# Optimization experiments

Hardware: AMD Instinct MI355X
Metric: run time of the kernel (lower is better)

The kernel has to match this reference:

```python
import jax, jax.numpy as jnp
import numpy as np

W_SIZE = 7      # window side
TOPK = 8        # top-k windows gathered per query window
D_HEAD = 32     # head dim
EPS = 1e-6      # linear-attention denominator eps


def _windows(x, ws):
    # x: [b, d, H, W] -> [b, (m*n), ws*ws, d]
    b, d, H, W = x.shape
    m, n = H // ws, W // ws
    x = x.reshape(b, d, m, ws, n, ws)
    return x.transpose(0, 2, 4, 3, 5, 1).reshape(b, m * n, ws * ws, d), m, n


def setup_inputs() -> dict:
    key = jax.random.key(0)
    kq, kk, kv = jax.random.split(key, 3)
    shape = (4, 256, 112, 112)
    return {
        "q": jax.random.normal(kq, shape, dtype=jnp.float32),
        "k": jax.random.normal(kk, shape, dtype=jnp.float32),
        "v": jax.random.normal(kv, shape, dtype=jnp.float32),
    }


def reference(q, k, v):
    b, d, H, W = q.shape
    ws = W_SIZE
    qw, m, n = _windows(q, ws)
    kw, _, _ = _windows(k, ws)
    vw, _, _ = _windows(v, ws)
    nw = m * n

    # window mean pooling
    qm = qw.mean(axis=2)  # [b, nw, d]
    km = kw.mean(axis=2)
    vm = vw.mean(axis=2)

    # coarse window similarity + topk
    sim = jnp.einsum('bmd,bnd->bmn', qm, km)
    _, idx = jax.lax.top_k(sim, TOPK)  # [b, nw, TOPK] int32

    # gather fine key/value windows: kw[i][idx[i]] -> [b, nw, TOPK, ws*ws, d]
    gather = jax.vmap(lambda w_, i_: w_[i_])
    fine_k = gather(kw, idx).reshape(b, nw, TOPK * ws * ws, d)
    fine_v = gather(vw, idx).reshape(b, nw, TOPK * ws * ws, d)

    # concat coarse (mean) tokens tiled across query windows
    keys = jnp.concatenate([fine_k, jnp.broadcast_to(km[:, None], (b, nw, nw, d))], axis=2)
    values = jnp.concatenate([fine_v, jnp.broadcast_to(vm[:, None], (b, nw, nw, d))], axis=2)

    h_heads = d // D_HEAD
    L = ws * ws
    S = keys.shape[2]
    Q = qw.reshape(b * nw, L, h_heads, D_HEAD)
    K = keys.reshape(b * nw, S, h_heads, D_HEAD)
    V = values.reshape(b * nw, S, h_heads, D_HEAD)

    # linear attention (elu feature map)
    Qf = jax.nn.elu(Q) + 1.0
    Kf = jax.nn.elu(K) + 1.0
    Vn = V / S
    KV = jnp.einsum('nshd,nshv->nhdv', Kf, Vn)
    Z = 1.0 / (jnp.einsum('nlhd,nhd->nlh', Qf, Kf.sum(axis=1)) + EPS)
    msg = jnp.einsum('nlhd,nhdv,nlh->nlhv', Qf, KV, Z) * S  # [b*nw, L, h, D_HEAD]

    # '(b m n) (w1 w2) h d -> b (h d) (m w1) (n w2)'
    msg = msg.reshape(b, m, n, ws, ws, h_heads, D_HEAD)
    msg = msg.transpose(0, 5, 6, 1, 3, 2, 4).reshape(b, d, m * ws, n * ws)
    return msg
```

## Files before the change

kernel.cpp:

```cpp
#include <hip/hip_runtime.h>
#include <float.h>

#define B 4
#define D 256
#define HH 112
#define WW 112
#define WS 7
#define NW 256
#define LL 49
#define TOPK 8
#define NH 8
#define DH 32
#define PADK 136
#define PADQ 136

typedef unsigned short u16;
typedef unsigned int u32;

__device__ __forceinline__ float elu1(float x) {
    return x > 0.f ? x + 1.f : __expf(x);
}
__device__ __forceinline__ float bf2f(u16 u) {
    return __uint_as_float(((u32)u) << 16);
}
__device__ __forceinline__ u16 f2bf(float x) {
    u32 u = __float_as_uint(x);
    u32 r = (u + 0x7FFFu + ((u >> 16) & 1u)) >> 16;
    return (u16)r;
}

__global__ __launch_bounds__(256) void k_xform(
        const float* __restrict__ q, const float* __restrict__ k,
        const float* __restrict__ v,
        u16* __restrict__ qwin, u16* __restrict__ kwin, u16* __restrict__ vwin,
        float* __restrict__ qm, float* __restrict__ kmf,
        float* __restrict__ vm, float* __restrict__ kmT) {
    __shared__ float stage[16 * 392];
    int blk = blockIdx.x;
    int cg = blk & 15, wjh = (blk >> 4) & 1, wi = (blk >> 5) & 15;
    int b = (blk >> 9) & 3, ti = blk >> 11;
    int c0 = cg * 16;
    int t = threadIdx.x;
    const float* src = ti == 0 ? q : (ti == 1 ? k : v);
    u16* dst = ti == 0 ? qwin : (ti == 1 ? kwin : vwin);

    for (int p = t; p < 1568; p += 256) {
        int c = p / 98;
        int f4 = (p - c * 98) * 4;
        int r = f4 / 56, lcol = f4 - r * 56;
        const float* gp = src +
            ((size_t)((b * D + c0 + c) * HH + wi * WS + r)) * WW + wjh * 56 + lcol;
        *(float4*)&stage[c * 392 + f4] = *(const float4*)gp;
    }
    __syncthreads();

    if (t < 128) {
        int c = t >> 3, wjl = t & 7;
        int base = c * 392 + wjl * 7;
        float s = 0.f;
        for (int r = 0; r < WS; ++r)
            for (int x = 0; x < WS; ++x)
                s += stage[base + r * 56 + x];
        float mean = s * (1.f / 49.f);
        int C = c0 + c;
        int win = wi * 16 + wjh * 8 + wjl;
        if (ti == 0) qm[(size_t)(b * NW + win) * D + C] = mean;
        else if (ti == 1) {
            kmf[(size_t)(b * NW + win) * D + C] = elu1(mean);
            kmT[(size_t)(b * D + C) * NW + win] = mean;
        } else vm[(size_t)(b * NW + win) * D + C] = mean;
    }
    __syncthreads();

    for (int p = t; p < 784; p += 256) {
        int wjl = p / 98;
        int rem = p - wjl * 98;
        int l = rem >> 1, oct = rem & 1;
        int r = l / 7, x = l - r * 7;
        int fo = r * 56 + wjl * 7 + x;
        u32 wds[4];
        for (int h = 0; h < 4; ++h) {
            int cA = oct * 8 + h * 2;
            u16 a  = f2bf(stage[cA * 392 + fo]);
            u16 bq = f2bf(stage[(cA + 1) * 392 + fo]);
            wds[h] = ((u32)bq << 16) | a;
        }
        int win = wi * 16 + wjh * 8 + wjl;
        u16* gp = dst + ((size_t)(b * NW + win) * LL + l) * D + c0 + oct * 8;
        *(uint4*)gp = make_uint4(wds[0], wds[1], wds[2], wds[3]);
    }
}

__global__ __launch_bounds__(256) void k_topk(
        const float* __restrict__ qm, const float* __restrict__ kmT,
        int* __restrict__ idx) {
    __shared__ float qrow[D];
    __shared__ float cval[4];
    __shared__ int cidx[4];
    __shared__ int winner;
    int b = blockIdx.x >> 8;
    int qw = blockIdx.x & 255;
    int t = threadIdx.x;
    qrow[t] = qm[(size_t)(b * NW + qw) * D + t];
    __syncthreads();
    const float* kb = kmT + (size_t)b * D * NW + t;
    float a0 = 0.f, a1 = 0.f, a2 = 0.f, a3 = 0.f;
    for (int d = 0; d < D; d += 4) {
        a0 += qrow[d]     * kb[(size_t)d * NW];
        a1 += qrow[d + 1] * kb[(size_t)(d + 1) * NW];
        a2 += qrow[d + 2] * kb[(size_t)(d + 2) * NW];
        a3 += qrow[d + 3] * kb[(size_t)(d + 3) * NW];
    }
    float val = (a0 + a1) + (a2 + a3);
    for (int sel = 0; sel < TOPK; ++sel) {
        float v = val; int ii = t;
        for (int off = 32; off > 0; off >>= 1) {
            float ov = __shfl_xor(v, off);
            int oi = __shfl_xor(ii, off);
            if (ov > v || (ov == v && oi < ii)) { v = ov; ii = oi; }
        }
        if ((t & 63) == 0) { cval[t >> 6] = v; cidx[t >> 6] = ii; }
        __syncthreads();
        if (t == 0) {
            float bv = cval[0]; int bi = cidx[0];
            for (int w = 1; w < 4; ++w)
                if (cval[w] > bv || (cval[w] == bv && cidx[w] < bi)) {
                    bv = cval[w]; bi = cidx[w];
                }
            idx[(size_t)(b * NW + qw) * TOPK + sel] = bi;
            winner = bi;
        }
        __syncthreads();
        if (t == winner) val = -FLT_MAX;
    }
}

__global__ __launch_bounds__(256) void k_kvw(
        const u16* __restrict__ kwin, const u16* __restrict__ vwin,
        float* __restrict__ KVw, float* __restrict__ Ksw) {
    __shared__ u16 kf[LL * PADK];
    __shared__ u16 vf[LL * PADK];
    int blk = blockIdx.x;
    int b = blk >> 9;
    int win = (blk >> 1) & 255;
    int half = blk & 1;
    int t = threadIdx.x;
    for (int p = t; p < 784; p += 256) {
        int l = p >> 4, oct = p & 15;
        size_t goff = ((size_t)(b * NW + win) * LL + l) * D + half * 128 + oct * 8;
        uint4 raw = *(const uint4*)(kwin + goff);
        u32 w[4] = {raw.x, raw.y, raw.z, raw.w};
        u32 o[4];
        for (int h = 0; h < 4; ++h) {
            float lo = elu1(__uint_as_float(w[h] << 16));
            float hi = elu1(__uint_as_float(w[h] & 0xffff0000u));
            o[h] = ((u32)f2bf(hi) << 16) | f2bf(lo);
        }
        *(uint4*)&kf[l * PADK + oct * 8] = make_uint4(o[0], o[1], o[2], o[3]);
        *(uint4*)&vf[l * PADK + oct * 8] = *(const uint4*)(vwin + goff);
    }
    __syncthreads();
    int h2 = t >> 6;
    int q64 = t & 63;
    int ddq = q64 >> 3, dvq = q64 & 7;
    int ab = h2 * 32 + ddq * 4;
    int bb = h2 * 32 + dvq * 4;
    float acc[4][4] = {};
    float ks[4] = {};
    for (int l = 0; l < LL; ++l) {
        uint2 kr = *(const uint2*)&kf[l * PADK + ab];
        uint2 vr = *(const uint2*)&vf[l * PADK + bb];
        float av[4] = {
            __uint_as_float(kr.x << 16), __uint_as_float(kr.x & 0xffff0000u),
            __uint_as_float(kr.y << 16), __uint_as_float(kr.y & 0xffff0000u)};
        float bw[4] = {
            __uint_as_float(vr.x << 16), __uint_as_float(vr.x & 0xffff0000u),
            __uint_as_float(vr.y << 16), __uint_as_float(vr.y & 0xffff0000u)};
        ks[0] += av[0]; ks[1] += av[1]; ks[2] += av[2]; ks[3] += av[3];
        for (int i = 0; i < 4; ++i)
            for (int j = 0; j < 4; ++j)
                acc[i][j] += av[i] * bw[j];
    }
    int h = half * 4 + h2;
    size_t obase = (size_t)((b * NW + win) * NH + h) * (DH * DH);
    for (int i = 0; i < 4; ++i) {
        float4 o = {acc[i][0], acc[i][1], acc[i][2], acc[i][3]};
        *(float4*)&KVw[obase + (size_t)(ddq * 4 + i) * DH + dvq * 4] = o;
    }
    if (dvq == 0) {
        float4 o = {ks[0], ks[1], ks[2], ks[3]};
        *(float4*)&Ksw[(size_t)((b * NW + win) * NH + h) * DH + ddq * 4] = o;
    }
}

__global__ __launch_bounds__(256) void k_kvc(
        const float* __restrict__ kmf, const float* __restrict__ vm,
        float* __restrict__ KVc, float* __restrict__ Ksc) {
    int b = blockIdx.x >> 1;
    int half = blockIdx.x & 1;
    int t = threadIdx.x;
    int h2 = t >> 6;
    int q64 = t & 63;
    int ddq = q64 >> 3, dvq = q64 & 7;
    int ca = half * 128 + h2 * 32 + ddq * 4;
    int cb = half * 128 + h2 * 32 + dvq * 4;
    const float* kb = kmf + (size_t)b * NW * D;
    const float* vb = vm + (size_t)b * NW * D;
    float acc[4][4] = {};
    float ks[4] = {};
#pragma unroll 4
    for (int n = 0; n < NW; ++n) {
        float4 a  = *(const float4*)&kb[n * D + ca];
        float4 bv = *(const float4*)&vb[n * D + cb];
        float av[4] = {a.x, a.y, a.z, a.w};
        float bw[4] = {bv.x, bv.y, bv.z, bv.w};
        ks[0] += av[0]; ks[1] += av[1]; ks[2] += av[2]; ks[3] += av[3];
        for (int i = 0; i < 4; ++i)
            for (int j = 0; j < 4; ++j)
                acc[i][j] += av[i] * bw[j];
    }
    int h = half * 4 + h2;
    size_t obase = (size_t)(b * NH + h) * (DH * DH);
    for (int i = 0; i < 4; ++i) {
        float4 o = {acc[i][0], acc[i][1], acc[i][2], acc[i][3]};
        *(float4*)&KVc[obase + (size_t)(ddq * 4 + i) * DH + dvq * 4] = o;
    }
    if (dvq == 0) {
        float4 o = {ks[0], ks[1], ks[2], ks[3]};
        *(float4*)&Ksc[(size_t)(b * NH + h) * DH + ddq * 4] = o;
    }
}

__global__ __launch_bounds__(256) void k_final(
        const u16* qwin, const int* __restrict__ idx,
        const float* __restrict__ KVw, const float* __restrict__ Ksw,
        const float* __restrict__ KVc, const float* __restrict__ Ksc,
        u16* msg) {
    __shared__ float kv[4 * DH * DH];
    __shared__ float ksl[4 * DH];
    __shared__ u16 qf[LL * PADQ];
    __shared__ int idxl[TOPK];
    int blk = blockIdx.x;
    int lin = ((blk & 7) << 8) | (blk >> 3);
    int half = lin & 1;
    int qw = (lin >> 1) & 255;
    int b = lin >> 9;
    int t = threadIdx.x;
    if (t < TOPK) idxl[t] = idx[(size_t)(b * NW + qw) * TOPK + t];
    for (int p = t; p < 784; p += 256) {
        int l = p >> 4, oct = p & 15;
        const u16* gp = qwin +
            ((size_t)(b * NW + qw) * LL + l) * D + half * 128 + oct * 8;
        uint4 raw = *(const uint4*)gp;
        u32 wsin[4] = {raw.x, raw.y, raw.z, raw.w};
        u32 wout[4];
        for (int h = 0; h < 4; ++h) {
            float lo = elu1(__uint_as_float(wsin[h] << 16));
            float hi = elu1(__uint_as_float(wsin[h] & 0xffff0000u));
            wout[h] = ((u32)f2bf(hi) << 16) | f2bf(lo);
        }
        *(uint4*)&qf[l * PADQ + oct * 8] = make_uint4(wout[0], wout[1], wout[2], wout[3]);
    }
    __syncthreads();
    {
        int h2 = t >> 6;
        int dd = (t & 63) >> 1;
        int dvh = t & 1;
        int h = half * 4 + h2;
        float kvacc[16] = {};
        float ksacc = 0.f;
        for (int s = 0; s <= TOPK; ++s) {
            const float* kvsrc;
            const float* kssrc;
            if (s < TOPK) {
                int srcw = idxl[s];
                kvsrc = KVw + (size_t)((b * NW + srcw) * NH + h) * (DH * DH);
                kssrc = Ksw + (size_t)((b * NW + srcw) * NH + h) * DH;
            } else {
                kvsrc = KVc + (size_t)(b * NH + h) * (DH * DH);
                kssrc = Ksc + (size_t)(b * NH + h) * DH;
            }
            const float* rowp = kvsrc + (size_t)dd * DH + dvh * 16;
            for (int j4 = 0; j4 < 4; ++j4) {
                float4 r4 = *(const float4*)&rowp[j4 * 4];
                kvacc[j4 * 4 + 0] += r4.x; kvacc[j4 * 4 + 1] += r4.y;
                kvacc[j4 * 4 + 2] += r4.z; kvacc[j4 * 4 + 3] += r4.w;
            }
            ksacc += kssrc[dd];
        }
        for (int j = 0; j < 16; ++j)
            kv[h2 * (DH * DH) + dd * DH + dvh * 16 + j] = kvacc[j];
        if (dvh == 0) ksl[h2 * DH + dd] = ksacc;
    }
    __syncthreads();
    {
        int lset = t >> 7;
        int h2 = (t >> 5) & 3;
        int dv = t & 31;
        float kvcol[DH], ksr[DH];
        for (int dd = 0; dd < DH; ++dd) {
            kvcol[dd] = kv[h2 * (DH * DH) + dd * DH + dv];
            ksr[dd]  = ksl[h2 * DH + dd];
        }
        int l0 = lset * 25;
        int l1 = l0 + 25; if (l1 > LL) l1 = LL;
        for (int l = l0; l < l1; ++l) {
            const u16* qrow = &qf[l * PADQ + h2 * DH];
            float m = 0.f, z = 0.f;
            for (int dd2 = 0; dd2 < 16; ++dd2) {
                u32 w = *(const u32*)&qrow[dd2 * 2];
                float q0 = __uint_as_float(w << 16);
                float q1 = __uint_as_float(w & 0xffff0000u);
                m += q0 * kvcol[2 * dd2] + q1 * kvcol[2 * dd2 + 1];
                z += q0 * ksr[2 * dd2] + q1 * ksr[2 * dd2 + 1];
            }
            qf[l * PADQ + h2 * DH + dv] = f2bf(m / (z + 1e-6f));
        }
    }
    __syncthreads();
    for (int p = t; p < 784; p += 256) {
        int l = p >> 4, oct = p & 15;
        uint4 w = *(const uint4*)&qf[l * PADQ + oct * 8];
        u16* gp = msg + ((size_t)(b * NW + qw) * LL + l) * D + half * 128 + oct * 8;
        *(uint4*)gp = w;
    }
}

__global__ __launch_bounds__(256) void k_out(
        const u16* __restrict__ msg, float* __restrict__ out) {
    __shared__ u16 ms[16 * LL * 32];
    int blk = blockIdx.x;
    int cg = blk & 7, wi = (blk >> 3) & 15, b = blk >> 7;
    int c0 = cg * 32;
    int t = threadIdx.x;
    for (int p = t; p < 3136; p += 256) {
        int wj = p / 196;
        int rem = p - wj * 196;
        int l = rem >> 2, oct = rem & 3;
        const u16* gp = msg +
            ((size_t)(b * NW + wi * 16 + wj) * LL + l) * D + c0 + oct * 8;
        uint4 raw = *(const uint4*)gp;
        *(uint4*)&ms[(wj * LL + l) * 32 + oct * 8] = raw;
    }
    __syncthreads();
    for (int p = t; p < 6272; p += 256) {
        int c = p / 196;
        int rem = p - c * 196;
        int f = rem * 4;
        int r = f / 112, col = f - r * 112;
        float4 o;
        float* op = (float*)&o;
        for (int j = 0; j < 4; ++j) {
            int xg = col + j;
            int wj = xg / 7, x = xg - wj * 7;
            int l = r * 7 + x;
            op[j] = bf2f(ms[(wj * LL + l) * 32 + c]);
        }
        float* gp = out + ((size_t)((b * D + c0 + c) * HH + wi * WS + r)) * WW + col;
        *(float4*)gp = o;
    }
}

extern "C" void kernel_launch(void* const* d_in, const int* in_sizes, int n_in,
                              void* d_out, int out_size, void* d_ws, size_t ws_size,
                              hipStream_t stream) {
    const float* q = (const float*)d_in[0];
    const float* k = (const float*)d_in[1];
    const float* v = (const float*)d_in[2];
    float* out = (float*)d_out;
    char* base = (char*)d_ws;

    float* qm  = (float*)(base);
    float* kmf = (float*)(base + (size_t)1 * (1 << 20));
    float* vm  = (float*)(base + (size_t)2 * (1 << 20));
    float* kmT = (float*)(base + (size_t)3 * (1 << 20));
    int*   idx = (int*)  (base + (size_t)4 * (1 << 20));
    float* Ksw = (float*)(base + (size_t)4 * (1 << 20) + (1 << 15));
    float* KVc = (float*)(base + (size_t)5 * (1 << 20) + (1 << 15));
    float* Ksc = (float*)(base + (size_t)5 * (1 << 20) + (1 << 15) + (1 << 17));
    float* KVw = (float*)(base + (size_t)6 * (1 << 20));
    u16* kwin  = (u16*)(base + (size_t)40 * (1 << 20));
    u16* vwin  = (u16*)(base + (size_t)65 * (1 << 20));
    u16* qwin  = (u16*)(base + (size_t)90 * (1 << 20));

    k_xform<<<dim3(3 * B * 16 * 2 * 16), dim3(256), 0, stream>>>(
        q, k, v, qwin, kwin, vwin, qm, kmf, vm, kmT);
    k_topk <<<dim3(B * NW), dim3(256), 0, stream>>>(qm, kmT, idx);
    k_kvw  <<<dim3(B * NW * 2), dim3(256), 0, stream>>>(kwin, vwin, KVw, Ksw);
    k_kvc  <<<dim3(B * 2), dim3(256), 0, stream>>>(kmf, vm, KVc, Ksc);
    k_final<<<dim3(B * NW * 2), dim3(256), 0, stream>>>(
        qwin, idx, KVw, Ksw, KVc, Ksc, qwin );
    k_out  <<<dim3(B * 16 * 8), dim3(256), 0, stream>>>(qwin, out);
}
```

Measured before the change: 381.5 us.

## Switch window buffers to channel-major layout, fold ELU into transform, merge coarse KV kernel

Window tensors are now stored channel-major ([win][channel][56 padded tokens]) instead of token-major. The ELU feature map is applied once in the transform kernel rather than being recomputed in the KV and final kernels. The coarse KV computation moves into extra blocks of the per-window KV kernel, removing one launch. Per-window KV matrices are stored in bf16 to cut gather traffic in the final kernel. Staging, the final matvec loop and the output scatter are reorganised around the new layout, which adds token padding and some bf16 rounding of the KV sums.

```diff
diff --git a/kernel.cpp b/kernel.cpp
--- a/kernel.cpp
+++ b/kernel.cpp
@@ -8,11 +8,11 @@
 #define WS 7
 #define NW 256
 #define LL 49
+#define LP 56
 #define TOPK 8
 #define NH 8
 #define DH 32
-#define PADK 136
-#define PADQ 136
+#define STK 60
 
 typedef unsigned short u16;
 typedef unsigned int u32;
@@ -28,6 +28,8 @@
     u32 r = (u + 0x7FFFu + ((u >> 16) & 1u)) >> 16;
     return (u16)r;
 }
+__device__ __forceinline__ float bflo(u32 w) { return __uint_as_float(w << 16); }
+__device__ __forceinline__ float bfhi(u32 w) { return __uint_as_float(w & 0xffff0000u); }
 
 __global__ __launch_bounds__(256) void k_xform(
         const float* __restrict__ q, const float* __restrict__ k,
@@ -35,35 +37,32 @@
         u16* __restrict__ qwin, u16* __restrict__ kwin, u16* __restrict__ vwin,
         float* __restrict__ qm, float* __restrict__ kmf,
         float* __restrict__ vm, float* __restrict__ kmT) {
-    __shared__ float stage[16 * 392];
+    __shared__ float stage[8 * 788];
     int blk = blockIdx.x;
-    int cg = blk & 15, wjh = (blk >> 4) & 1, wi = (blk >> 5) & 15;
-    int b = (blk >> 9) & 3, ti = blk >> 11;
-    int c0 = cg * 16;
+    int cg = blk & 31, wi = (blk >> 5) & 15, b = (blk >> 9) & 3, ti = blk >> 11;
+    int c0 = cg * 8;
     int t = threadIdx.x;
     const float* src = ti == 0 ? q : (ti == 1 ? k : v);
     u16* dst = ti == 0 ? qwin : (ti == 1 ? kwin : vwin);
 
     for (int p = t; p < 1568; p += 256) {
-        int c = p / 98;
-        int f4 = (p - c * 98) * 4;
-        int r = f4 / 56, lcol = f4 - r * 56;
-        const float* gp = src +
-            ((size_t)((b * D + c0 + c) * HH + wi * WS + r)) * WW + wjh * 56 + lcol;
-        *(float4*)&stage[c * 392 + f4] = *(const float4*)gp;
+        int c = p / 196;
+        int i4 = (p - c * 196) * 4;
+        const float* gp = src + (size_t)(b * D + c0 + c) * (HH * WW) + wi * 784 + i4;
+        *(float4*)&stage[c * 788 + i4] = *(const float4*)gp;
     }
     __syncthreads();
 
     if (t < 128) {
-        int c = t >> 3, wjl = t & 7;
-        int base = c * 392 + wjl * 7;
+        int c = t >> 4, wjl = t & 15;
+        int base = c * 788 + wjl * 7;
         float s = 0.f;
         for (int r = 0; r < WS; ++r)
             for (int x = 0; x < WS; ++x)
-                s += stage[base + r * 56 + x];
+                s += stage[base + r * 112 + x];
         float mean = s * (1.f / 49.f);
         int C = c0 + c;
-        int win = wi * 16 + wjh * 8 + wjl;
+        int win = wi * 16 + wjl;
         if (ti == 0) qm[(size_t)(b * NW + win) * D + C] = mean;
         else if (ti == 1) {
             kmf[(size_t)(b * NW + win) * D + C] = elu1(mean);
@@ -72,22 +71,25 @@
     }
     __syncthreads();
 
-    for (int p = t; p < 784; p += 256) {
-        int wjl = p / 98;
-        int rem = p - wjl * 98;
-        int l = rem >> 1, oct = rem & 1;
-        int r = l / 7, x = l - r * 7;
-        int fo = r * 56 + wjl * 7 + x;
-        u32 wds[4];
-        for (int h = 0; h < 4; ++h) {
-            int cA = oct * 8 + h * 2;
-            u16 a  = f2bf(stage[cA * 392 + fo]);
-            u16 bq = f2bf(stage[(cA + 1) * 392 + fo]);
-            wds[h] = ((u32)bq << 16) | a;
-        }
-        int win = wi * 16 + wjh * 8 + wjl;
-        u16* gp = dst + ((size_t)(b * NW + win) * LL + l) * D + c0 + oct * 8;
-        *(uint4*)gp = make_uint4(wds[0], wds[1], wds[2], wds[3]);
+    for (int p = t; p < 896; p += 256) {
+        int wjl = p / 56;
+        int rem = p - wjl * 56;
+        int c = rem / 7, j = rem % 7;
+        u16 vals[8];
+        for (int i = 0; i < 8; ++i) {
+            int l = j * 8 + i;
+            if (l < LL) {
+                int r = l / 7, x = l - r * 7;
+                float f = stage[c * 788 + r * 112 + wjl * 7 + x];
+                if (ti < 2) f = elu1(f);
+                vals[i] = f2bf(f);
+            } else vals[i] = 0;
+        }
+        int win = wi * 16 + wjl;
+        u16* gp = dst + ((size_t)(b * NW + win) * D + c0 + c) * LP + j * 8;
+        *(uint4*)gp = make_uint4(
+            ((u32)vals[1] << 16) | vals[0], ((u32)vals[3] << 16) | vals[2],
+            ((u32)vals[5] << 16) | vals[4], ((u32)vals[7] << 16) | vals[6]);
     }
 }
 
@@ -137,55 +139,88 @@
 
 __global__ __launch_bounds__(256) void k_kvw(
         const u16* __restrict__ kwin, const u16* __restrict__ vwin,
-        float* __restrict__ KVw, float* __restrict__ Ksw) {
-    __shared__ u16 kf[LL * PADK];
-    __shared__ u16 vf[LL * PADK];
+        const float* __restrict__ kmf, const float* __restrict__ vm,
+        u16* __restrict__ KVw, float* __restrict__ Ksw,
+        float* __restrict__ KVc, float* __restrict__ Ksc) {
+    __shared__ u16 kf[128 * STK];
+    __shared__ u16 vf[128 * STK];
     int blk = blockIdx.x;
+    int t = threadIdx.x;
+    if (blk >= B * NW * 2) {
+        int blkc = blk - B * NW * 2;
+        int b = blkc >> 1, half = blkc & 1;
+        int h2 = t >> 6, q64 = t & 63, ddq = q64 >> 3, dvq = q64 & 7;
+        int ca = half * 128 + h2 * 32 + ddq * 4;
+        int cb = half * 128 + h2 * 32 + dvq * 4;
+        const float* kb = kmf + (size_t)b * NW * D;
+        const float* vb = vm + (size_t)b * NW * D;
+        float acc[4][4] = {};
+        float ks[4] = {};
+        for (int n = 0; n < NW; ++n) {
+            float4 a  = *(const float4*)&kb[n * D + ca];
+            float4 bv = *(const float4*)&vb[n * D + cb];
+            float av[4] = {a.x, a.y, a.z, a.w};
+            float bw[4] = {bv.x, bv.y, bv.z, bv.w};
+            ks[0] += av[0]; ks[1] += av[1]; ks[2] += av[2]; ks[3] += av[3];
+            for (int i = 0; i < 4; ++i)
+                for (int j = 0; j < 4; ++j)
+                    acc[i][j] += av[i] * bw[j];
+        }
+        int h = half * 4 + h2;
+        size_t obase = (size_t)(b * NH + h) * (DH * DH);
+        for (int i = 0; i < 4; ++i) {
+            float4 o = {acc[i][0], acc[i][1], acc[i][2], acc[i][3]};
+            *(float4*)&KVc[obase + (size_t)(ddq * 4 + i) * DH + dvq * 4] = o;
+        }
+        if (dvq == 0) {
+            float4 o = {ks[0], ks[1], ks[2], ks[3]};
+            *(float4*)&Ksc[(size_t)(b * NH + h) * DH + ddq * 4] = o;
+        }
+        return;
+    }
     int b = blk >> 9;
     int win = (blk >> 1) & 255;
     int half = blk & 1;
-    int t = threadIdx.x;
-    for (int p = t; p < 784; p += 256) {
-        int l = p >> 4, oct = p & 15;
-        size_t goff = ((size_t)(b * NW + win) * LL + l) * D + half * 128 + oct * 8;
-        uint4 raw = *(const uint4*)(kwin + goff);
-        u32 w[4] = {raw.x, raw.y, raw.z, raw.w};
-        u32 o[4];
-        for (int h = 0; h < 4; ++h) {
-            float lo = elu1(__uint_as_float(w[h] << 16));
-            float hi = elu1(__uint_as_float(w[h] & 0xffff0000u));
-            o[h] = ((u32)f2bf(hi) << 16) | f2bf(lo);
-        }
-        *(uint4*)&kf[l * PADK + oct * 8] = make_uint4(o[0], o[1], o[2], o[3]);
-        *(uint4*)&vf[l * PADK + oct * 8] = *(const uint4*)(vwin + goff);
-    }
-    __syncthreads();
-    int h2 = t >> 6;
-    int q64 = t & 63;
-    int ddq = q64 >> 3, dvq = q64 & 7;
-    int ab = h2 * 32 + ddq * 4;
-    int bb = h2 * 32 + dvq * 4;
+    const u16* kg = kwin + ((size_t)(b * NW + win) * D + half * 128) * LP;
+    const u16* vg = vwin + ((size_t)(b * NW + win) * D + half * 128) * LP;
+    for (int p = t; p < 896; p += 256) {
+        int c = p / 7, j = p % 7;
+        uint4 kq = *(const uint4*)(kg + c * LP + j * 8);
+        uint4 vq = *(const uint4*)(vg + c * LP + j * 8);
+        *(uint2*)&kf[c * STK + j * 8]     = make_uint2(kq.x, kq.y);
+        *(uint2*)&kf[c * STK + j * 8 + 4] = make_uint2(kq.z, kq.w);
+        *(uint2*)&vf[c * STK + j * 8]     = make_uint2(vq.x, vq.y);
+        *(uint2*)&vf[c * STK + j * 8 + 4] = make_uint2(vq.z, vq.w);
+    }
+    __syncthreads();
+    int h2 = t >> 6, q64 = t & 63, ddq = q64 >> 3, dvq = q64 & 7;
+    const u16* ka = kf + (h2 * 32 + ddq * 4) * STK;
+    const u16* vb = vf + (h2 * 32 + dvq * 4) * STK;
     float acc[4][4] = {};
     float ks[4] = {};
-    for (int l = 0; l < LL; ++l) {
-        uint2 kr = *(const uint2*)&kf[l * PADK + ab];
-        uint2 vr = *(const uint2*)&vf[l * PADK + bb];
-        float av[4] = {
-            __uint_as_float(kr.x << 16), __uint_as_float(kr.x & 0xffff0000u),
-            __uint_as_float(kr.y << 16), __uint_as_float(kr.y & 0xffff0000u)};
-        float bw[4] = {
-            __uint_as_float(vr.x << 16), __uint_as_float(vr.x & 0xffff0000u),
-            __uint_as_float(vr.y << 16), __uint_as_float(vr.y & 0xffff0000u)};
-        ks[0] += av[0]; ks[1] += av[1]; ks[2] += av[2]; ks[3] += av[3];
-        for (int i = 0; i < 4; ++i)
+    for (int l4 = 0; l4 < 14; ++l4) {
+        float a[4][4], w[4][4];
+        for (int i = 0; i < 4; ++i) {
+            uint2 kr = *(const uint2*)(ka + i * STK + l4 * 4);
+            a[i][0] = bflo(kr.x); a[i][1] = bfhi(kr.x);
+            a[i][2] = bflo(kr.y); a[i][3] = bfhi(kr.y);
+            uint2 vr = *(const uint2*)(vb + i * STK + l4 * 4);
+            w[i][0] = bflo(vr.x); w[i][1] = bfhi(vr.x);
+            w[i][2] = bflo(vr.y); w[i][3] = bfhi(vr.y);
+        }
+        for (int i = 0; i < 4; ++i) {
+            ks[i] += (a[i][0] + a[i][1]) + (a[i][2] + a[i][3]);
             for (int j = 0; j < 4; ++j)
-                acc[i][j] += av[i] * bw[j];
+                for (int s = 0; s < 4; ++s)
+                    acc[i][j] += a[i][s] * w[j][s];
+        }
     }
     int h = half * 4 + h2;
-    size_t obase = (size_t)((b * NW + win) * NH + h) * (DH * DH);
+    u16* ob = KVw + (size_t)((b * NW + win) * NH + h) * (DH * DH);
     for (int i = 0; i < 4; ++i) {
-        float4 o = {acc[i][0], acc[i][1], acc[i][2], acc[i][3]};
-        *(float4*)&KVw[obase + (size_t)(ddq * 4 + i) * DH + dvq * 4] = o;
+        u32 p0 = ((u32)f2bf(acc[i][1]) << 16) | f2bf(acc[i][0]);
+        u32 p1 = ((u32)f2bf(acc[i][3]) << 16) | f2bf(acc[i][2]);
+        *(uint2*)(ob + (ddq * 4 + i) * DH + dvq * 4) = make_uint2(p0, p1);
     }
     if (dvq == 0) {
         float4 o = {ks[0], ks[1], ks[2], ks[3]};
@@ -193,52 +228,14 @@
     }
 }
 
-__global__ __launch_bounds__(256) void k_kvc(
-        const float* __restrict__ kmf, const float* __restrict__ vm,
-        float* __restrict__ KVc, float* __restrict__ Ksc) {
-    int b = blockIdx.x >> 1;
-    int half = blockIdx.x & 1;
-    int t = threadIdx.x;
-    int h2 = t >> 6;
-    int q64 = t & 63;
-    int ddq = q64 >> 3, dvq = q64 & 7;
-    int ca = half * 128 + h2 * 32 + ddq * 4;
-    int cb = half * 128 + h2 * 32 + dvq * 4;
-    const float* kb = kmf + (size_t)b * NW * D;
-    const float* vb = vm + (size_t)b * NW * D;
-    float acc[4][4] = {};
-    float ks[4] = {};
-#pragma unroll 4
-    for (int n = 0; n < NW; ++n) {
-        float4 a  = *(const float4*)&kb[n * D + ca];
-        float4 bv = *(const float4*)&vb[n * D + cb];
-        float av[4] = {a.x, a.y, a.z, a.w};
-        float bw[4] = {bv.x, bv.y, bv.z, bv.w};
-        ks[0] += av[0]; ks[1] += av[1]; ks[2] += av[2]; ks[3] += av[3];
-        for (int i = 0; i < 4; ++i)
-            for (int j = 0; j < 4; ++j)
-                acc[i][j] += av[i] * bw[j];
-    }
-    int h = half * 4 + h2;
-    size_t obase = (size_t)(b * NH + h) * (DH * DH);
-    for (int i = 0; i < 4; ++i) {
-        float4 o = {acc[i][0], acc[i][1], acc[i][2], acc[i][3]};
-        *(float4*)&KVc[obase + (size_t)(ddq * 4 + i) * DH + dvq * 4] = o;
-    }
-    if (dvq == 0) {
-        float4 o = {ks[0], ks[1], ks[2], ks[3]};
-        *(float4*)&Ksc[(size_t)(b * NH + h) * DH + ddq * 4] = o;
-    }
-}
-
 __global__ __launch_bounds__(256) void k_final(
         const u16* qwin, const int* __restrict__ idx,
-        const float* __restrict__ KVw, const float* __restrict__ Ksw,
+        const u16* __restrict__ KVw, const float* __restrict__ Ksw,
         const float* __restrict__ KVc, const float* __restrict__ Ksc,
         u16* msg) {
     __shared__ float kv[4 * DH * DH];
     __shared__ float ksl[4 * DH];
-    __shared__ u16 qf[LL * PADQ];
+    __shared__ u16 qf[128 * LP];
     __shared__ int idxl[TOPK];
     int blk = blockIdx.x;
     int lin = ((blk & 7) << 8) | (blk >> 3);
@@ -247,20 +244,9 @@
     int b = lin >> 9;
     int t = threadIdx.x;
     if (t < TOPK) idxl[t] = idx[(size_t)(b * NW + qw) * TOPK + t];
-    for (int p = t; p < 784; p += 256) {
-        int l = p >> 4, oct = p & 15;
-        const u16* gp = qwin +
-            ((size_t)(b * NW + qw) * LL + l) * D + half * 128 + oct * 8;
-        uint4 raw = *(const uint4*)gp;
-        u32 wsin[4] = {raw.x, raw.y, raw.z, raw.w};
-        u32 wout[4];
-        for (int h = 0; h < 4; ++h) {
-            float lo = elu1(__uint_as_float(wsin[h] << 16));
-            float hi = elu1(__uint_as_float(wsin[h] & 0xffff0000u));
-            wout[h] = ((u32)f2bf(hi) << 16) | f2bf(lo);
-        }
-        *(uint4*)&qf[l * PADQ + oct * 8] = make_uint4(wout[0], wout[1], wout[2], wout[3]);
-    }
+    const u16* qg = qwin + ((size_t)(b * NW + qw) * D + half * 128) * LP;
+    for (int p = t; p < 896; p += 256)
+        *(uint4*)&qf[p * 8] = *(const uint4*)(qg + p * 8);
     __syncthreads();
     {
         int h2 = t >> 6;
@@ -269,24 +255,33 @@
         int h = half * 4 + h2;
         float kvacc[16] = {};
         float ksacc = 0.f;
-        for (int s = 0; s <= TOPK; ++s) {
-            const float* kvsrc;
-            const float* kssrc;
-            if (s < TOPK) {
-                int srcw = idxl[s];
-                kvsrc = KVw + (size_t)((b * NW + srcw) * NH + h) * (DH * DH);
-                kssrc = Ksw + (size_t)((b * NW + srcw) * NH + h) * DH;
-            } else {
-                kvsrc = KVc + (size_t)(b * NH + h) * (DH * DH);
-                kssrc = Ksc + (size_t)(b * NH + h) * DH;
+        for (int s = 0; s < TOPK; ++s) {
+            int srcw = idxl[s];
+            const u16* rp = KVw + (size_t)((b * NW + srcw) * NH + h) * (DH * DH)
+                            + dd * DH + dvh * 16;
+            uint4 r0 = *(const uint4*)rp;
+            uint4 r1 = *(const uint4*)(rp + 8);
+            u32 wsv[4] = {r0.x, r0.y, r0.z, r0.w};
+            for (int h4 = 0; h4 < 4; ++h4) {
+                kvacc[h4 * 2]     += bflo(wsv[h4]);
+                kvacc[h4 * 2 + 1] += bfhi(wsv[h4]);
             }
-            const float* rowp = kvsrc + (size_t)dd * DH + dvh * 16;
+            u32 wsv1[4] = {r1.x, r1.y, r1.z, r1.w};
+            for (int h4 = 0; h4 < 4; ++h4) {
+                kvacc[8 + h4 * 2]     += bflo(wsv1[h4]);
+                kvacc[8 + h4 * 2 + 1] += bfhi(wsv1[h4]);
+            }
+            ksacc += Ksw[(size_t)((b * NW + srcw) * NH + h) * DH + dd];
+        }
+        {
+            const float* rowp = KVc + (size_t)(b * NH + h) * (DH * DH)
+                                + dd * DH + dvh * 16;
             for (int j4 = 0; j4 < 4; ++j4) {
                 float4 r4 = *(const float4*)&rowp[j4 * 4];
                 kvacc[j4 * 4 + 0] += r4.x; kvacc[j4 * 4 + 1] += r4.y;
                 kvacc[j4 * 4 + 2] += r4.z; kvacc[j4 * 4 + 3] += r4.w;
             }
-            ksacc += kssrc[dd];
+            ksacc += Ksc[(size_t)(b * NH + h) * DH + dd];
         }
         for (int j = 0; j < 16; ++j)
             kv[h2 * (DH * DH) + dd * DH + dvh * 16 + j] = kvacc[j];
@@ -297,66 +292,74 @@
         int lset = t >> 7;
         int h2 = (t >> 5) & 3;
         int dv = t & 31;
-        float kvcol[DH], ksr[DH];
+        int l0 = lset * 28;
+        float m[28] = {}, z[28] = {};
         for (int dd = 0; dd < DH; ++dd) {
-            kvcol[dd] = kv[h2 * (DH * DH) + dd * DH + dv];
-            ksr[dd]  = ksl[h2 * DH + dd];
-        }
-        int l0 = lset * 25;
-        int l1 = l0 + 25; if (l1 > LL) l1 = LL;
-        for (int l = l0; l < l1; ++l) {
-            const u16* qrow = &qf[l * PADQ + h2 * DH];
-            float m = 0.f, z = 0.f;
-            for (int dd2 = 0; dd2 < 16; ++dd2) {
-                u32 w = *(const u32*)&qrow[dd2 * 2];
-                float q0 = __uint_as_float(w << 16);
-                float q1 = __uint_as_float(w & 0xffff0000u);
-                m += q0 * kvcol[2 * dd2] + q1 * kvcol[2 * dd2 + 1];
-                z += q0 * ksr[2 * dd2] + q1 * ksr[2 * dd2 + 1];
+            float kc = kv[h2 * (DH * DH) + dd * DH + dv];
+            float ko = ksl[h2 * DH + dd];
+            const u16* qr = qf + (h2 * 32 + dd) * LP + l0;
+#pragma unroll
+            for (int u = 0; u < 7; ++u) {
+                uint2 qq = *(const uint2*)(qr + u * 4);
+                float q0 = bflo(qq.x), q1 = bfhi(qq.x);
+                float q2 = bflo(qq.y), q3 = bfhi(qq.y);
+                m[u * 4 + 0] += q0 * kc; z[u * 4 + 0] += q0 * ko;
+                m[u * 4 + 1] += q1 * kc; z[u * 4 + 1] += q1 * ko;
+                m[u * 4 + 2] += q2 * kc; z[u * 4 + 2] += q2 * ko;
+                m[u * 4 + 3] += q3 * kc; z[u * 4 + 3] += q3 * ko;
             }
-            qf[l * PADQ + h2 * DH + dv] = f2bf(m / (z + 1e-6f));
-        }
-    }
-    __syncthreads();
-    for (int p = t; p < 784; p += 256) {
-        int l = p >> 4, oct = p & 15;
-        uint4 w = *(const uint4*)&qf[l * PADQ + oct * 8];
-        u16* gp = msg + ((size_t)(b * NW + qw) * LL + l) * D + half * 128 + oct * 8;
-        *(uint4*)gp = w;
+        }
+        u16 r[28];
+#pragma unroll
+        for (int l = 0; l < 28; ++l)
+            r[l] = f2bf(m[l] / (z[l] + 1e-6f));
+        int C = half * 128 + h2 * 32 + dv;
+        u16* mg = msg + ((size_t)(b * NW + qw) * D + C) * LP + l0;
+        if (lset == 0) {
+            for (int u = 0; u < 7; ++u)
+                *(uint2*)(mg + u * 4) = make_uint2(
+                    ((u32)r[u * 4 + 1] << 16) | r[u * 4],
+                    ((u32)r[u * 4 + 3] << 16) | r[u * 4 + 2]);
+        } else {
+            for (int u = 0; u < 5; ++u)
+                *(uint2*)(mg + u * 4) = make_uint2(
+                    ((u32)r[u * 4 + 1] << 16) | r[u * 4],
+                    ((u32)r[u * 4 + 3] << 16) | r[u * 4 + 2]);
+            mg[20] = r[20];
+        }
     }
 }
 
 __global__ __launch_bounds__(256) void k_out(
         const u16* __restrict__ msg, float* __restrict__ out) {
-    __shared__ u16 ms[16 * LL * 32];
+    __shared__ u16 ms[16 * 16 * LP];
     int blk = blockIdx.x;
-    int cg = blk & 7, wi = (blk >> 3) & 15, b = blk >> 7;
-    int c0 = cg * 32;
-    int t = threadIdx.x;
+    int cg = blk & 15, wi = (blk >> 4) & 15, b = blk >> 8;
+    int c0 = cg * 16;
+    int t = threadIdx.x;
+    for (int p = t; p < 1792; p += 256) {
+        int wjl = p / 112;
+        int rem = p - wjl * 112;
+        int c = rem / 7, j = rem % 7;
+        const u16* gp = msg +
+            ((size_t)(b * NW + wi * 16 + wjl) * D + c0 + c) * LP + j * 8;
+        *(uint4*)&ms[(wjl * 16 + c) * LP + j * 8] = *(const uint4*)gp;
+    }
+    __syncthreads();
     for (int p = t; p < 3136; p += 256) {
-        int wj = p / 196;
-        int rem = p - wj * 196;
-        int l = rem >> 2, oct = rem & 3;
-        const u16* gp = msg +
-            ((size_t)(b * NW + wi * 16 + wj) * LL + l) * D + c0 + oct * 8;
-        uint4 raw = *(const uint4*)gp;
-        *(uint4*)&ms[(wj * LL + l) * 32 + oct * 8] = raw;
-    }
-    __syncthreads();
-    for (int p = t; p < 6272; p += 256) {
         int c = p / 196;
-        int rem = p - c * 196;
-        int f = rem * 4;
-        int r = f / 112, col = f - r * 112;
+        int f4 = (p - c * 196) * 4;
+        int r = f4 / 112, col = f4 - r * 112;
         float4 o;
         float* op = (float*)&o;
         for (int j = 0; j < 4; ++j) {
             int xg = col + j;
             int wj = xg / 7, x = xg - wj * 7;
             int l = r * 7 + x;
-            op[j] = bf2f(ms[(wj * LL + l) * 32 + c]);
-        }
-        float* gp = out + ((size_t)((b * D + c0 + c) * HH + wi * WS + r)) * WW + col;
+            op[j] = bf2f(ms[(wj * 16 + c) * LP + l]);
+        }
+        float* gp = out + (size_t)(b * D + c0 + c) * (HH * WW)
+                    + (wi * WS + r) * WW + col;
         *(float4*)gp = o;
     }
 }
@@ -370,25 +373,26 @@
     float* out = (float*)d_out;
     char* base = (char*)d_ws;
 
+    const size_t MB = 1 << 20;
     float* qm  = (float*)(base);
-    float* kmf = (float*)(base + (size_t)1 * (1 << 20));
-    float* vm  = (float*)(base + (size_t)2 * (1 << 20));
-    float* kmT = (float*)(base + (size_t)3 * (1 << 20));
-    int*   idx = (int*)  (base + (size_t)4 * (1 << 20));
-    float* Ksw = (float*)(base + (size_t)4 * (1 << 20) + (1 << 15));
-    float* KVc = (float*)(base + (size_t)5 * (1 << 20) + (1 << 15));
-    float* Ksc = (float*)(base + (size_t)5 * (1 << 20) + (1 << 15) + (1 << 17));
-    float* KVw = (float*)(base + (size_t)6 * (1 << 20));
-    u16* kwin  = (u16*)(base + (size_t)40 * (1 << 20));
-    u16* vwin  = (u16*)(base + (size_t)65 * (1 << 20));
-    u16* qwin  = (u16*)(base + (size_t)90 * (1 << 20));
-
-    k_xform<<<dim3(3 * B * 16 * 2 * 16), dim3(256), 0, stream>>>(
+    float* kmf = (float*)(base + 1 * MB);
+    float* vm  = (float*)(base + 2 * MB);
+    float* kmT = (float*)(base + 3 * MB);
+    int*   idx = (int*)  (base + 4 * MB);
+    float* Ksw = (float*)(base + 4 * MB + (1 << 15));
+    float* KVc = (float*)(base + 5 * MB + (1 << 15));
+    float* Ksc = (float*)(base + 5 * MB + (1 << 15) + (1 << 17));
+    u16* KVw  = (u16*)(base + 6 * MB);
+    u16* kwin = (u16*)(base + 24 * MB);
+    u16* vwin = (u16*)(base + 52 * MB);
+    u16* qwin = (u16*)(base + 80 * MB);
+
+    k_xform<<<dim3(3 * B * 16 * 32), dim3(256), 0, stream>>>(
         q, k, v, qwin, kwin, vwin, qm, kmf, vm, kmT);
     k_topk <<<dim3(B * NW), dim3(256), 0, stream>>>(qm, kmT, idx);
-    k_kvw  <<<dim3(B * NW * 2), dim3(256), 0, stream>>>(kwin, vwin, KVw, Ksw);
-    k_kvc  <<<dim3(B * 2), dim3(256), 0, stream>>>(kmf, vm, KVc, Ksc);
+    k_kvw  <<<dim3(B * NW * 2 + B * 2), dim3(256), 0, stream>>>(
+        kwin, vwin, kmf, vm, KVw, Ksw, KVc, Ksc);
     k_final<<<dim3(B * NW * 2), dim3(256), 0, stream>>>(
         qwin, idx, KVw, Ksw, KVc, Ksc, qwin );
-    k_out  <<<dim3(B * 16 * 8), dim3(256), 0, stream>>>(qwin, out);
-}
+    k_out  <<<dim3(B * 16 * 16), dim3(256), 0, stream>>>(qwin, out);
+}
```

Result: faster. 319.2 us (-16.3%).
